# Kernel tuning notes

Hardware: AMD Instinct MI355X
Metric: run time of the kernel (lower is better)

The kernel has to match this reference:

```python
import jax, jax.numpy as jnp
import numpy as np

B, S, OBS, ZD, HID, T, PD = 256, 512, 64, 16, 256, 64, 2
ITERS, ELITES = 4, 64
SMOOTH, STD_FLOOR = 0.25, 0.2
IW, AW, RW = 1.0, 0.5, 1.0


def setup_inputs() -> dict:
    key = jax.random.key(0)
    ks = jax.random.split(key, 32)
    f32 = jnp.float32

    def w(k, shape):
        return jax.random.normal(k, shape, f32) / np.float32(np.sqrt(shape[0]))

    return {
        "s0": jax.random.normal(ks[0], (B, OBS), f32),
        "eps": jax.random.normal(ks[1], (ITERS, B, S, ZD), f32),
        "enc_w1": w(ks[2], (OBS, HID)), "enc_b1": jnp.zeros((HID,), f32),
        "enc_w2": w(ks[3], (HID, HID)), "enc_b2": jnp.zeros((HID,), f32),
        "zmu_w": w(ks[4], (HID, ZD)), "zmu_b": jnp.zeros((ZD,), f32),
        "zls_w": w(ks[5], (HID, ZD)), "zls_b": jnp.zeros((ZD,), f32),
        "mu_w1": w(ks[6], (OBS + ZD, HID)), "mu_b1": jnp.zeros((HID,), f32),
        "mu_w2": w(ks[7], (HID, HID)), "mu_b2": jnp.zeros((HID,), f32),
        "mu_w3": w(ks[8], (HID, T * PD)), "mu_b3": jnp.zeros((T * PD,), f32),
        "sig_w1": w(ks[9], (ZD, HID)), "sig_b1": jnp.zeros((HID,), f32),
        "sig_w2": w(ks[10], (HID, HID)), "sig_b2": jnp.zeros((HID,), f32),
        "sig_w3": w(ks[11], (HID, T * PD)), "sig_b3": jnp.zeros((T * PD,), f32),  # bias zero-init per nn.init.zeros_
        "risk_w1": w(ks[12], (OBS + ZD, HID)), "risk_b1": jnp.zeros((HID,), f32),
        "risk_w2": w(ks[13], (HID, HID)), "risk_b2": jnp.zeros((HID,), f32),
        "risk_w3": w(ks[14], (HID, 1)), "risk_b3": jnp.zeros((1,), f32),
    }


def _cem_bind(s0, eps, enc_w1, enc_b1, enc_w2, enc_b2, zmu_w, zmu_b, zls_w, zls_b,
              mu_w1, mu_b1, mu_w2, mu_b2, mu_w3, mu_b3,
              sig_w1, sig_b1, sig_w2, sig_b2, sig_w3, sig_b3,
              risk_w1, risk_b1, risk_w2, risk_b2, risk_w3, risk_b3):
    relu = jax.nn.relu
    b, obs = s0.shape
    iters, _, s, zd = eps.shape

    # --- TubeNet.encode: q(z|s0) ---
    h = relu(s0 @ enc_w1 + enc_b1)
    h = relu(h @ enc_w2 + enc_b2)
    mu = h @ zmu_w + zmu_b                                   # [B, ZD]
    std = jnp.exp(jnp.clip(h @ zls_w + zls_b, -4.0, 2.0))    # [B, ZD]

    goal = s0[:, 2:4]                                        # extract_goal
    s0e = jnp.broadcast_to(s0[:, None, :], (b, s, obs))      # [B, S, OBS]

    best_score = jnp.full((b,), -jnp.inf, dtype=s0.dtype)
    best_z = mu

    for i in range(iters):  # small fixed CEM iteration count
        z = mu[:, None, :] + std[:, None, :] * eps[i]        # [B, S, ZD]
        x = jnp.concatenate([s0e, z], axis=-1)               # [B, S, OBS+ZD]

        # predict_tube: mu_net(s0, z)
        hm = relu(x @ mu_w1 + mu_b1)
        hm = relu(hm @ mu_w2 + mu_b2)
        mu_out = (hm @ mu_w3 + mu_b3).reshape(b, s, T, PD)

        # sigma_net(z), clamp(-4, 3); agency = -mean(log sigma) = -mean(logsig)
        hs = relu(z @ sig_w1 + sig_b1)
        hs = relu(hs @ sig_w2 + sig_b2)
        logsig = jnp.clip(hs @ sig_w3 + sig_b3, -4.0, 3.0)   # [B, S, T*PD]

        # intent proxy: ||mu_T - goal||^2
        intent = jnp.sum((mu_out[:, :, -1, :] - goal[:, None, :]) ** 2, axis=-1)  # [B, S]
        agency = -jnp.mean(logsig, axis=-1)                  # [B, S]

        # RiskNet(s0, z)
        hr = relu(x @ risk_w1 + risk_b1)
        hr = relu(hr @ risk_w2 + risk_b2)
        risk = jax.nn.sigmoid(hr @ risk_w3 + risk_b3)[..., 0]  # [B, S]

        score = -IW * intent + AW * agency - RW * risk       # [B, S]

        vals, idx = jax.lax.top_k(score, ELITES)             # [B, E]
        elite_z = jnp.take_along_axis(z, idx[:, :, None], axis=1)  # [B, E, ZD]

        better = vals[:, 0] > best_score
        top_z = jnp.take_along_axis(z, idx[:, :1, None], axis=1)[:, 0, :]
        best_score = jnp.where(better, vals[:, 0], best_score)
        best_z = jnp.where(better[:, None], top_z, best_z)

        new_mu = elite_z.mean(axis=1)
        new_std = jnp.std(elite_z, axis=1, ddof=1)           # torch .std default (unbiased)
        mu = SMOOTH * mu + (1.0 - SMOOTH) * new_mu
        std = jnp.maximum(SMOOTH * std + (1.0 - SMOOTH) * new_std, STD_FLOOR)

    return jnp.concatenate([best_z, best_score[:, None]], axis=-1)  # [B, ZD+1]


def reference(s0, eps, enc_w1, enc_b1, enc_w2, enc_b2, zmu_w, zmu_b, zls_w, zls_b,
              mu_w1, mu_b1, mu_w2, mu_b2, mu_w3, mu_b3,
              sig_w1, sig_b1, sig_w2, sig_b2, sig_w3, sig_b3,
              risk_w1, risk_b1, risk_w2, risk_b2, risk_w3, risk_b3):
    return _cem_bind(s0, eps, enc_w1, enc_b1, enc_w2, enc_b2, zmu_w, zmu_b, zls_w, zls_b,
                     mu_w1, mu_b1, mu_w2, mu_b2, mu_w3, mu_b3,
                     sig_w1, sig_b1, sig_w2, sig_b2, sig_w3, sig_b3,
                     risk_w1, risk_b1, risk_w2, risk_b2, risk_w3, risk_b3)
```

## Files before the change

kernel.cpp:

```cpp
#include <hip/hip_runtime.h>

#define B_    256
#define S_    512
#define OBS_  64
#define ZD_   16
#define HID_  256
#define ITERS_ 4
#define RT_   64
#define STRH_ 68

__global__ __launch_bounds__(256) void enc_kernel(
    const float* __restrict__ s0,
    const float* __restrict__ w1, const float* __restrict__ b1,
    const float* __restrict__ w2, const float* __restrict__ b2,
    const float* __restrict__ zmw, const float* __restrict__ zmb,
    const float* __restrict__ zlw, const float* __restrict__ zlb,
    const float* __restrict__ mu_w1, const float* __restrict__ mu_b1,
    const float* __restrict__ risk_w1, const float* __restrict__ risk_b1,
    float* __restrict__ mu, float* __restrict__ stdv, float* __restrict__ bscore,
    float* __restrict__ base_mu, float* __restrict__ base_risk)
{
    __shared__ float s0s[OBS_];
    __shared__ float h1[HID_];
    __shared__ float h2[HID_];
    const int b = blockIdx.x, tid = threadIdx.x;
    if (tid < OBS_) s0s[tid] = s0[b * OBS_ + tid];
    __syncthreads();
    {
        float am = mu_b1[tid], ar = risk_b1[tid];
        for (int k = 0; k < OBS_; ++k) {
            am = fmaf(s0s[k], mu_w1[k * 256 + tid], am);
            ar = fmaf(s0s[k], risk_w1[k * 256 + tid], ar);
        }
        base_mu[b * 256 + tid]   = am;
        base_risk[b * 256 + tid] = ar;
    }
    float a = b1[tid];
    for (int k = 0; k < OBS_; ++k) a = fmaf(s0s[k], w1[k * HID_ + tid], a);
    h1[tid] = fmaxf(a, 0.f);
    __syncthreads();
    float a2 = b2[tid];
    for (int k = 0; k < HID_; ++k) a2 = fmaf(h1[k], w2[k * HID_ + tid], a2);
    h2[tid] = fmaxf(a2, 0.f);
    __syncthreads();
    if (tid < ZD_) {
        float m = zmb[tid];
        for (int k = 0; k < HID_; ++k) m = fmaf(h2[k], zmw[k * ZD_ + tid], m);
        mu[b * ZD_ + tid] = m;
    } else if (tid < 2 * ZD_) {
        const int d = tid - ZD_;
        float l = zlb[d];
        for (int k = 0; k < HID_; ++k) l = fmaf(h2[k], zlw[k * ZD_ + d], l);
        l = fminf(fmaxf(l, -4.f), 2.f);
        stdv[b * ZD_ + d] = expf(l);
    } else if (tid == 2 * ZD_) {
        bscore[b] = -INFINITY;
    }
}

__device__ __forceinline__ void fma32x2(
    const float* __restrict__ row, float wx, float wy,
    float* __restrict__ acc0, float* __restrict__ acc1)
{
#pragma unroll
    for (int s = 0; s < 4; ++s) {
        const float4 a0 = *(const float4*)(row + 8 * s);
        const float4 a1 = *(const float4*)(row + 8 * s + 4);
        const float aa[8] = {a0.x,a0.y,a0.z,a0.w, a1.x,a1.y,a1.z,a1.w};
#pragma unroll
        for (int r = 0; r < 8; ++r) {
            acc0[8*s+r] = fmaf(aa[r], wx, acc0[8*s+r]);
            acc1[8*s+r] = fmaf(aa[r], wy, acc1[8*s+r]);
        }
    }
}

__device__ __forceinline__ void fma32x1(
    const float* __restrict__ row, float w, float* __restrict__ acc)
{
#pragma unroll
    for (int s = 0; s < 4; ++s) {
        const float4 a0 = *(const float4*)(row + 8 * s);
        const float4 a1 = *(const float4*)(row + 8 * s + 4);
        const float aa[8] = {a0.x,a0.y,a0.z,a0.w, a1.x,a1.y,a1.z,a1.w};
#pragma unroll
        for (int r = 0; r < 8; ++r) acc[8*s+r] = fmaf(aa[r], w, acc[8*s+r]);
    }
}

__device__ __forceinline__ void gemm_k2(
    const float* __restrict__ inS, int K,
    const float* __restrict__ wcol,
    float* __restrict__ acc0, float* __restrict__ acc1)
{
    float2 wA[4], wB[4];
#pragma unroll
    for (int i = 0; i < 4; ++i) wA[i] = *(const float2*)(wcol + (size_t)i * 256);
#pragma unroll 1
    for (int k0 = 0; k0 < K; k0 += 8) {
#pragma unroll
        for (int i = 0; i < 4; ++i)
            wB[i] = *(const float2*)(wcol + (size_t)(k0 + 4 + i) * 256);
#pragma unroll
        for (int i = 0; i < 4; ++i)
            fma32x2(inS + (k0 + i) * STRH_, wA[i].x, wA[i].y, acc0, acc1);
        if (k0 + 8 < K) {
#pragma unroll
            for (int i = 0; i < 4; ++i)
                wA[i] = *(const float2*)(wcol + (size_t)(k0 + 8 + i) * 256);
        }
#pragma unroll
        for (int i = 0; i < 4; ++i)
            fma32x2(inS + (k0 + 4 + i) * STRH_, wB[i].x, wB[i].y, acc0, acc1);
    }
}

__device__ __forceinline__ void gemm_k1(
    const float* __restrict__ inS, int K,
    const float* __restrict__ wcol, int wstride, float* __restrict__ acc)
{
    float wA[4], wB[4];
#pragma unroll
    for (int i = 0; i < 4; ++i) wA[i] = wcol[(size_t)i * wstride];
#pragma unroll 1
    for (int k0 = 0; k0 < K; k0 += 8) {
#pragma unroll
        for (int i = 0; i < 4; ++i) wB[i] = wcol[(size_t)(k0 + 4 + i) * wstride];
#pragma unroll
        for (int i = 0; i < 4; ++i) fma32x1(inS + (k0 + i) * STRH_, wA[i], acc);
        if (k0 + 8 < K) {
#pragma unroll
            for (int i = 0; i < 4; ++i) wA[i] = wcol[(size_t)(k0 + 8 + i) * wstride];
        }
#pragma unroll
        for (int i = 0; i < 4; ++i) fma32x1(inS + (k0 + 4 + i) * STRH_, wB[i], acc);
    }
}

__device__ __forceinline__ void store32_relu(float* __restrict__ dst, int c,
                                             int g32, const float* __restrict__ acc)
{
#pragma unroll
    for (int q = 0; q < 8; ++q) {
        float4 o;
        o.x = fmaxf(acc[4*q+0], 0.f); o.y = fmaxf(acc[4*q+1], 0.f);
        o.z = fmaxf(acc[4*q+2], 0.f); o.w = fmaxf(acc[4*q+3], 0.f);
        *(float4*)(dst + (size_t)c * STRH_ + g32 + 4*q) = o;
    }
}

__global__ __launch_bounds__(256, 2) void score_kernel(
    const float* __restrict__ s0, const float* __restrict__ eps,
    const float* __restrict__ mu_w1,
    const float* __restrict__ mu_w2, const float* __restrict__ mu_b2,
    const float* __restrict__ mu_w3, const float* __restrict__ mu_b3,
    const float* __restrict__ sig_w1, const float* __restrict__ sig_b1,
    const float* __restrict__ sig_w2, const float* __restrict__ sig_b2,
    const float* __restrict__ sig_w3, const float* __restrict__ sig_b3,
    const float* __restrict__ risk_w1,
    const float* __restrict__ risk_w2, const float* __restrict__ risk_b2,
    const float* __restrict__ risk_w3, const float* __restrict__ risk_b3,
    const float* __restrict__ base_mu, const float* __restrict__ base_risk,
    const float* __restrict__ mu, const float* __restrict__ stdv,
    float* __restrict__ score, int iter)
{
    __shared__ __align__(16) float zT[ZD_ * STRH_];
    __shared__ __align__(16) float h[HID_ * STRH_];
    __shared__ float red[4][RT_], red2[4][RT_];
    __shared__ float intentL[RT_], agencyL[RT_];
    __shared__ float muS[ZD_], stdS[ZD_];

    const int tid  = threadIdx.x;
    const int g    = tid >> 7;
    const int g32  = g * 32;
    const int c0   = (tid & 127) * 2;
    const int row0 = blockIdx.x * RT_;
    const int b    = row0 >> 9;

    if (tid < ZD_) { muS[tid] = mu[b * ZD_ + tid]; stdS[tid] = stdv[b * ZD_ + tid]; }
    __syncthreads();
    {
        const float* epsI = eps + ((size_t)iter * B_ * S_ + row0) * ZD_;
        for (int l = tid; l < RT_ * ZD_; l += 256) {
            const int r = l >> 4, d = l & 15;
            zT[d * STRH_ + r] = fmaf(stdS[d], epsI[l], muS[d]);
        }
    }
    __syncthreads();

    float acc0[32], acc1[32];

    {
        const float2 bm = *(const float2*)(base_mu + (size_t)b * 256 + c0);
#pragma unroll
        for (int r = 0; r < 32; ++r) { acc0[r] = bm.x; acc1[r] = bm.y; }
        gemm_k2(zT + g32, ZD_, mu_w1 + (size_t)OBS_ * 256 + c0, acc0, acc1);
        store32_relu(h, c0, g32, acc0); store32_relu(h, c0 + 1, g32, acc1);
    }
    __syncthreads();
    {
        const float2 bv = *(const float2*)(mu_b2 + c0);
#pragma unroll
        for (int r = 0; r < 32; ++r) { acc0[r] = bv.x; acc1[r] = bv.y; }
        gemm_k2(h + g32, HID_, mu_w2 + c0, acc0, acc1);
    }
    __syncthreads();
    store32_relu(h, c0, g32, acc0); store32_relu(h, c0 + 1, g32, acc1);
    __syncthreads();
    {
        const int r = tid & 63, seg = tid >> 6;
        float p0 = 0.f, p1 = 0.f;
        for (int i = 0; i < 64; ++i) {
            const int k = seg * 64 + i;
            const float hv = h[k * STRH_ + r];
            const float2 wv = *(const float2*)(mu_w3 + (size_t)k * 128 + 126);
            p0 = fmaf(hv, wv.x, p0);
            p1 = fmaf(hv, wv.y, p1);
        }
        red[seg][r] = p0; red2[seg][r] = p1;
    }
    {
        const float2 bv = *(const float2*)(sig_b1 + c0);
#pragma unroll
        for (int r = 0; r < 32; ++r) { acc0[r] = bv.x; acc1[r] = bv.y; }
        gemm_k2(zT + g32, ZD_, sig_w1 + c0, acc0, acc1);
    }
    __syncthreads();
    store32_relu(h, c0, g32, acc0); store32_relu(h, c0 + 1, g32, acc1);
    if (tid < RT_) {
        float m0 = red[0][tid] + red[1][tid] + red[2][tid] + red[3][tid] + mu_b3[126];
        float m1 = red2[0][tid] + red2[1][tid] + red2[2][tid] + red2[3][tid] + mu_b3[127];
        const float g0 = s0[b * OBS_ + 2], g1 = s0[b * OBS_ + 3];
        const float d0 = m0 - g0, d1 = m1 - g1;
        intentL[tid] = d0 * d0 + d1 * d1;
    }
    __syncthreads();
    {
        const float2 bv = *(const float2*)(sig_b2 + c0);
#pragma unroll
        for (int r = 0; r < 32; ++r) { acc0[r] = bv.x; acc1[r] = bv.y; }
        gemm_k2(h + g32, HID_, sig_w2 + c0, acc0, acc1);
    }
    __syncthreads();
    store32_relu(h, c0, g32, acc0); store32_relu(h, c0 + 1, g32, acc1);
    __syncthreads();
    {
        const int c = tid & 127;
        float acc[32];
        const float bv = sig_b3[c];
#pragma unroll
        for (int r = 0; r < 32; ++r) acc[r] = bv;
        gemm_k1(h + g32, HID_, sig_w3 + c, 128, acc);
        __syncthreads();
#pragma unroll
        for (int q = 0; q < 8; ++q) {
            float4 o;
            o.x = fminf(fmaxf(acc[4*q+0], -4.f), 3.f);
            o.y = fminf(fmaxf(acc[4*q+1], -4.f), 3.f);
            o.z = fminf(fmaxf(acc[4*q+2], -4.f), 3.f);
            o.w = fminf(fmaxf(acc[4*q+3], -4.f), 3.f);
            *(float4*)(h + (size_t)c * STRH_ + g32 + 4*q) = o;
        }
    }
    __syncthreads();
    {
        const int r = tid & 63, seg = tid >> 6;
        float s = 0.f;
        for (int i = 0; i < 32; ++i) s += h[(seg * 32 + i) * STRH_ + r];
        red[seg][r] = s;
    }
    {
        const float2 bm = *(const float2*)(base_risk + (size_t)b * 256 + c0);
#pragma unroll
        for (int r = 0; r < 32; ++r) { acc0[r] = bm.x; acc1[r] = bm.y; }
        gemm_k2(zT + g32, ZD_, risk_w1 + (size_t)OBS_ * 256 + c0, acc0, acc1);
    }
    __syncthreads();
    store32_relu(h, c0, g32, acc0); store32_relu(h, c0 + 1, g32, acc1);
    if (tid < RT_) {
        const float s = red[0][tid] + red[1][tid] + red[2][tid] + red[3][tid];
        agencyL[tid] = -s * (1.f / 128.f);
    }
    __syncthreads();
    {
        const float2 bv = *(const float2*)(risk_b2 + c0);
#pragma unroll
        for (int r = 0; r < 32; ++r) { acc0[r] = bv.x; acc1[r] = bv.y; }
        gemm_k2(h + g32, HID_, risk_w2 + c0, acc0, acc1);
    }
    __syncthreads();
    store32_relu(h, c0, g32, acc0); store32_relu(h, c0 + 1, g32, acc1);
    __syncthreads();
    {
        const int r = tid & 63, seg = tid >> 6;
        float p = 0.f;
        for (int i = 0; i < 64; ++i) {
            const int k = seg * 64 + i;
            p = fmaf(h[k * STRH_ + r], risk_w3[k], p);
        }
        red[seg][r] = p;
    }
    __syncthreads();
    if (tid < RT_) {
        const float p = red[0][tid] + red[1][tid] + red[2][tid] + red[3][tid];
        const float risk = 1.f / (1.f + expf(-(p + risk_b3[0])));
        score[row0 + tid] = -intentL[tid] + 0.5f * agencyL[tid] - risk;
    }
}

__global__ __launch_bounds__(256) void update_kernel(
    const float* __restrict__ score, const float* __restrict__ eps,
    float* __restrict__ mu, float* __restrict__ stdv,
    float* __restrict__ bscore, float* __restrict__ bz, int iter)
{
    __shared__ unsigned long long keys[512];
    __shared__ float ez[64][ZD_];
    __shared__ float mold[ZD_], sold[ZD_];
    __shared__ int flagL, idx0L;

    const int b = blockIdx.x, tid = threadIdx.x;

    for (int l = tid; l < 512; l += 256) {
        const float sc = score[b * 512 + l];
        unsigned int u = __float_as_uint(sc);
        u = (u & 0x80000000u) ? ~u : (u | 0x80000000u);
        const unsigned long long key =
            ((unsigned long long)u << 32) | (unsigned long long)(511 - l);
        keys[l] = ~key;
    }
    if (tid < ZD_) { mold[tid] = mu[b * ZD_ + tid]; sold[tid] = stdv[b * ZD_ + tid]; }
    __syncthreads();

    for (int size = 2; size < 512; size <<= 1) {
        const int ddd = ((tid & (size >> 1)) != 0) ? 0 : 1;
        for (int stride = size >> 1; stride > 0; stride >>= 1) {
            __syncthreads();
            const int pos = 2 * tid - (tid & (stride - 1));
            const unsigned long long a = keys[pos], c = keys[pos + stride];
            if ((a > c) == (ddd != 0)) { keys[pos] = c; keys[pos + stride] = a; }
        }
    }
    for (int stride = 256; stride > 0; stride >>= 1) {
        __syncthreads();
        const int pos = 2 * tid - (tid & (stride - 1));
        const unsigned long long a = keys[pos], c = keys[pos + stride];
        if (a > c) { keys[pos] = c; keys[pos + stride] = a; }
    }
    __syncthreads();

    const float* epsB = eps + ((size_t)iter * B_ * S_ + (size_t)b * S_) * ZD_;
    for (int l = tid; l < 64 * ZD_; l += 256) {
        const int e = l >> 4, d = l & 15;
        const unsigned long long key = ~keys[e];
        const int idx = 511 - (int)(key & 0xFFFFFFFFull);
        ez[e][d] = fmaf(sold[d], epsB[idx * ZD_ + d], mold[d]);
    }
    __syncthreads();

    if (tid < ZD_) {
        float s = 0.f;
        for (int e = 0; e < 64; ++e) s += ez[e][tid];
        const float mean = s * (1.f / 64.f);
        float v = 0.f;
        for (int e = 0; e < 64; ++e) { const float d = ez[e][tid] - mean; v = fmaf(d, d, v); }
        const float sd = sqrtf(v * (1.f / 63.f));
        mu[b * ZD_ + tid]   = 0.25f * mold[tid] + 0.75f * mean;
        stdv[b * ZD_ + tid] = fmaxf(0.25f * sold[tid] + 0.75f * sd, 0.2f);
    }
    if (tid == 0) {
        const unsigned long long key = ~keys[0];
        const int idx0 = 511 - (int)(key & 0xFFFFFFFFull);
        const float v = score[b * 512 + idx0];
        const int better = (v > bscore[b]) ? 1 : 0;
        if (better) bscore[b] = v;
        flagL = better; idx0L = idx0;
    }
    __syncthreads();
    if (tid < ZD_ && flagL)
        bz[b * ZD_ + tid] = fmaf(sold[tid], epsB[idx0L * ZD_ + tid], mold[tid]);
}

__global__ __launch_bounds__(256) void out_kernel(
    const float* __restrict__ bz, const float* __restrict__ bscore,
    float* __restrict__ out)
{
    const int i = blockIdx.x * 256 + threadIdx.x;
    if (i < B_ * 17) {
        const int b = i / 17, d = i % 17;
        out[i] = (d < ZD_) ? bz[b * ZD_ + d] : bscore[b];
    }
}

extern "C" void kernel_launch(void* const* d_in, const int* in_sizes, int n_in,
                              void* d_out, int out_size, void* d_ws, size_t ws_size,
                              hipStream_t stream)
{
    (void)in_sizes; (void)n_in; (void)out_size; (void)ws_size;
    const float* s0      = (const float*)d_in[0];
    const float* eps     = (const float*)d_in[1];
    const float* enc_w1  = (const float*)d_in[2];
    const float* enc_b1  = (const float*)d_in[3];
    const float* enc_w2  = (const float*)d_in[4];
    const float* enc_b2  = (const float*)d_in[5];
    const float* zmu_w   = (const float*)d_in[6];
    const float* zmu_b   = (const float*)d_in[7];
    const float* zls_w   = (const float*)d_in[8];
    const float* zls_b   = (const float*)d_in[9];
    const float* mu_w1   = (const float*)d_in[10];
    const float* mu_b1   = (const float*)d_in[11];
    const float* mu_w2   = (const float*)d_in[12];
    const float* mu_b2   = (const float*)d_in[13];
    const float* mu_w3   = (const float*)d_in[14];
    const float* mu_b3   = (const float*)d_in[15];
    const float* sig_w1  = (const float*)d_in[16];
    const float* sig_b1  = (const float*)d_in[17];
    const float* sig_w2  = (const float*)d_in[18];
    const float* sig_b2  = (const float*)d_in[19];
    const float* sig_w3  = (const float*)d_in[20];
    const float* sig_b3  = (const float*)d_in[21];
    const float* risk_w1 = (const float*)d_in[22];
    const float* risk_b1 = (const float*)d_in[23];
    const float* risk_w2 = (const float*)d_in[24];
    const float* risk_b2 = (const float*)d_in[25];
    const float* risk_w3 = (const float*)d_in[26];
    const float* risk_b3 = (const float*)d_in[27];

    float* ws        = (float*)d_ws;
    float* mu        = ws;
    float* stdv      = ws + 4096;
    float* bscore    = ws + 8192;
    float* bz        = ws + 8448;
    float* score     = ws + 12544;
    float* base_mu   = ws + 143616;
    float* base_risk = ws + 209152;

    enc_kernel<<<B_, 256, 0, stream>>>(s0, enc_w1, enc_b1, enc_w2, enc_b2,
                                       zmu_w, zmu_b, zls_w, zls_b,
                                       mu_w1, mu_b1, risk_w1, risk_b1,
                                       mu, stdv, bscore, base_mu, base_risk);
    for (int it = 0; it < ITERS_; ++it) {
        score_kernel<<<(B_ * S_) / RT_, 256, 0, stream>>>(
            s0, eps,
            mu_w1, mu_w2, mu_b2, mu_w3, mu_b3,
            sig_w1, sig_b1, sig_w2, sig_b2, sig_w3, sig_b3,
            risk_w1, risk_w2, risk_b2, risk_w3, risk_b3,
            base_mu, base_risk,
            mu, stdv, score, it);
        update_kernel<<<B_, 256, 0, stream>>>(score, eps, mu, stdv, bscore, bz, it);
    }
    out_kernel<<<(B_ * 17 + 255) / 256, 256, 0, stream>>>(bz, bscore,
                                                          (float*)d_out);
}
```

Measured before the change: 3.207 ms.

## Retile score kernel GEMMs to 8x8 register blocks per thread

Changes each thread's register tile in the score MLP GEMMs from 32 rows by 2 columns to 8 rows by 8 columns, and the last sigma layer from 32x1 to 8x4. This balances shared-memory activation reads against global weight reads, and weights are now loaded as float4. It also stages the mu_w3 goal columns and risk_w3 in shared memory instead of re-reading them from global memory in the reduction loops. The cost is different LDS access patterns, with eight row groups now reading the same h rows, and possibly a changed register footprint.

New measurement: 3.107 ms. -3.1%, faster.

```diff
diff --git a/kernel.cpp b/kernel.cpp
--- a/kernel.cpp
+++ b/kernel.cpp
@@ -58,94 +58,106 @@
     }
 }
 
-__device__ __forceinline__ void fma32x2(
-    const float* __restrict__ row, float wx, float wy,
-    float* __restrict__ acc0, float* __restrict__ acc1)
-{
-#pragma unroll
-    for (int s = 0; s < 4; ++s) {
-        const float4 a0 = *(const float4*)(row + 8 * s);
-        const float4 a1 = *(const float4*)(row + 8 * s + 4);
-        const float aa[8] = {a0.x,a0.y,a0.z,a0.w, a1.x,a1.y,a1.z,a1.w};
-#pragma unroll
-        for (int r = 0; r < 8; ++r) {
-            acc0[8*s+r] = fmaf(aa[r], wx, acc0[8*s+r]);
-            acc1[8*s+r] = fmaf(aa[r], wy, acc1[8*s+r]);
-        }
-    }
-}
-
-__device__ __forceinline__ void fma32x1(
-    const float* __restrict__ row, float w, float* __restrict__ acc)
-{
-#pragma unroll
-    for (int s = 0; s < 4; ++s) {
-        const float4 a0 = *(const float4*)(row + 8 * s);
-        const float4 a1 = *(const float4*)(row + 8 * s + 4);
-        const float aa[8] = {a0.x,a0.y,a0.z,a0.w, a1.x,a1.y,a1.z,a1.w};
-#pragma unroll
-        for (int r = 0; r < 8; ++r) acc[8*s+r] = fmaf(aa[r], w, acc[8*s+r]);
-    }
-}
-
-__device__ __forceinline__ void gemm_k2(
+__device__ __forceinline__ void fma8x8(
+    const float* __restrict__ row, const float4 w0, const float4 w1,
+    float acc[8][8])
+{
+    const float4 q0 = *(const float4*)(row);
+    const float4 q1 = *(const float4*)(row + 4);
+    const float aa[8] = {q0.x,q0.y,q0.z,q0.w, q1.x,q1.y,q1.z,q1.w};
+    const float ww[8] = {w0.x,w0.y,w0.z,w0.w, w1.x,w1.y,w1.z,w1.w};
+#pragma unroll
+    for (int c = 0; c < 8; ++c)
+#pragma unroll
+        for (int r = 0; r < 8; ++r)
+            acc[c][r] = fmaf(aa[r], ww[c], acc[c][r]);
+}
+
+__device__ __forceinline__ void fma8x4(
+    const float* __restrict__ row, const float4 w0, float acc[4][8])
+{
+    const float4 q0 = *(const float4*)(row);
+    const float4 q1 = *(const float4*)(row + 4);
+    const float aa[8] = {q0.x,q0.y,q0.z,q0.w, q1.x,q1.y,q1.z,q1.w};
+    const float ww[4] = {w0.x,w0.y,w0.z,w0.w};
+#pragma unroll
+    for (int c = 0; c < 4; ++c)
+#pragma unroll
+        for (int r = 0; r < 8; ++r)
+            acc[c][r] = fmaf(aa[r], ww[c], acc[c][r]);
+}
+
+__device__ __forceinline__ void gemm_k8(
     const float* __restrict__ inS, int K,
-    const float* __restrict__ wcol,
-    float* __restrict__ acc0, float* __restrict__ acc1)
-{
-    float2 wA[4], wB[4];
-#pragma unroll
-    for (int i = 0; i < 4; ++i) wA[i] = *(const float2*)(wcol + (size_t)i * 256);
+    const float* __restrict__ wcol, float acc[8][8])
+{
+    float4 wA[4][2], wB[4][2];
+#pragma unroll
+    for (int i = 0; i < 4; ++i) {
+        wA[i][0] = *(const float4*)(wcol + (size_t)i * 256);
+        wA[i][1] = *(const float4*)(wcol + (size_t)i * 256 + 4);
+    }
 #pragma unroll 1
     for (int k0 = 0; k0 < K; k0 += 8) {
 #pragma unroll
+        for (int i = 0; i < 4; ++i) {
+            wB[i][0] = *(const float4*)(wcol + (size_t)(k0 + 4 + i) * 256);
+            wB[i][1] = *(const float4*)(wcol + (size_t)(k0 + 4 + i) * 256 + 4);
+        }
+#pragma unroll
         for (int i = 0; i < 4; ++i)
-            wB[i] = *(const float2*)(wcol + (size_t)(k0 + 4 + i) * 256);
+            fma8x8(inS + (k0 + i) * STRH_, wA[i][0], wA[i][1], acc);
+        if (k0 + 8 < K) {
+#pragma unroll
+            for (int i = 0; i < 4; ++i) {
+                wA[i][0] = *(const float4*)(wcol + (size_t)(k0 + 8 + i) * 256);
+                wA[i][1] = *(const float4*)(wcol + (size_t)(k0 + 8 + i) * 256 + 4);
+            }
+        }
 #pragma unroll
         for (int i = 0; i < 4; ++i)
-            fma32x2(inS + (k0 + i) * STRH_, wA[i].x, wA[i].y, acc0, acc1);
-        if (k0 + 8 < K) {
-#pragma unroll
-            for (int i = 0; i < 4; ++i)
-                wA[i] = *(const float2*)(wcol + (size_t)(k0 + 8 + i) * 256);
-        }
-#pragma unroll
-        for (int i = 0; i < 4; ++i)
-            fma32x2(inS + (k0 + 4 + i) * STRH_, wB[i].x, wB[i].y, acc0, acc1);
-    }
-}
-
-__device__ __forceinline__ void gemm_k1(
+            fma8x8(inS + (k0 + 4 + i) * STRH_, wB[i][0], wB[i][1], acc);
+    }
+}
+
+__device__ __forceinline__ void gemm_l3(
     const float* __restrict__ inS, int K,
-    const float* __restrict__ wcol, int wstride, float* __restrict__ acc)
-{
-    float wA[4], wB[4];
-#pragma unroll
-    for (int i = 0; i < 4; ++i) wA[i] = wcol[(size_t)i * wstride];
+    const float* __restrict__ wcol, float acc[4][8])
+{
+    float4 wA[4], wB[4];
+#pragma unroll
+    for (int i = 0; i < 4; ++i) wA[i] = *(const float4*)(wcol + (size_t)i * 128);
 #pragma unroll 1
     for (int k0 = 0; k0 < K; k0 += 8) {
 #pragma unroll
-        for (int i = 0; i < 4; ++i) wB[i] = wcol[(size_t)(k0 + 4 + i) * wstride];
-#pragma unroll
-        for (int i = 0; i < 4; ++i) fma32x1(inS + (k0 + i) * STRH_, wA[i], acc);
+        for (int i = 0; i < 4; ++i)
+            wB[i] = *(const float4*)(wcol + (size_t)(k0 + 4 + i) * 128);
+#pragma unroll
+        for (int i = 0; i < 4; ++i)
+            fma8x4(inS + (k0 + i) * STRH_, wA[i], acc);
         if (k0 + 8 < K) {
 #pragma unroll
-            for (int i = 0; i < 4; ++i) wA[i] = wcol[(size_t)(k0 + 8 + i) * wstride];
-        }
-#pragma unroll
-        for (int i = 0; i < 4; ++i) fma32x1(inS + (k0 + 4 + i) * STRH_, wB[i], acc);
-    }
-}
-
-__device__ __forceinline__ void store32_relu(float* __restrict__ dst, int c,
-                                             int g32, const float* __restrict__ acc)
-{
-#pragma unroll
-    for (int q = 0; q < 8; ++q) {
-        float4 o;
-        o.x = fmaxf(acc[4*q+0], 0.f); o.y = fmaxf(acc[4*q+1], 0.f);
-        o.z = fmaxf(acc[4*q+2], 0.f); o.w = fmaxf(acc[4*q+3], 0.f);
-        *(float4*)(dst + (size_t)c * STRH_ + g32 + 4*q) = o;
+            for (int i = 0; i < 4; ++i)
+                wA[i] = *(const float4*)(wcol + (size_t)(k0 + 8 + i) * 128);
+        }
+#pragma unroll
+        for (int i = 0; i < 4; ++i)
+            fma8x4(inS + (k0 + 4 + i) * STRH_, wB[i], acc);
+    }
+}
+
+__device__ __forceinline__ void store8x8_relu(float* __restrict__ dst, int c0,
+                                              int g8, const float acc[8][8])
+{
+#pragma unroll
+    for (int c = 0; c < 8; ++c) {
+#pragma unroll
+        for (int q = 0; q < 2; ++q) {
+            float4 o;
+            o.x = fmaxf(acc[c][4*q+0], 0.f); o.y = fmaxf(acc[c][4*q+1], 0.f);
+            o.z = fmaxf(acc[c][4*q+2], 0.f); o.w = fmaxf(acc[c][4*q+3], 0.f);
+            *(float4*)(dst + (size_t)(c0 + c) * STRH_ + g8 + 4*q) = o;
+        }
     }
 }
 
@@ -166,18 +178,26 @@
 {
     __shared__ __align__(16) float zT[ZD_ * STRH_];
     __shared__ __align__(16) float h[HID_ * STRH_];
+    __shared__ float w3m[2 * HID_];
+    __shared__ float rw3[HID_];
     __shared__ float red[4][RT_], red2[4][RT_];
     __shared__ float intentL[RT_], agencyL[RT_];
     __shared__ float muS[ZD_], stdS[ZD_];
 
     const int tid  = threadIdx.x;
-    const int g    = tid >> 7;
-    const int g32  = g * 32;
-    const int c0   = (tid & 127) * 2;
+    const int g    = tid >> 5;
+    const int g8   = g * 8;
+    const int ct   = tid & 31;
+    const int c0   = ct * 8;
     const int row0 = blockIdx.x * RT_;
     const int b    = row0 >> 9;
 
     if (tid < ZD_) { muS[tid] = mu[b * ZD_ + tid]; stdS[tid] = stdv[b * ZD_ + tid]; }
+    {
+        const float2 v = *(const float2*)(mu_w3 + (size_t)tid * 128 + 126);
+        w3m[2 * tid] = v.x; w3m[2 * tid + 1] = v.y;
+        rw3[tid] = risk_w3[tid];
+    }
     __syncthreads();
     {
         const float* epsI = eps + ((size_t)iter * B_ * S_ + row0) * ZD_;
@@ -188,24 +208,32 @@
     }
     __syncthreads();
 
-    float acc0[32], acc1[32];
-
-    {
-        const float2 bm = *(const float2*)(base_mu + (size_t)b * 256 + c0);
-#pragma unroll
-        for (int r = 0; r < 32; ++r) { acc0[r] = bm.x; acc1[r] = bm.y; }
-        gemm_k2(zT + g32, ZD_, mu_w1 + (size_t)OBS_ * 256 + c0, acc0, acc1);
-        store32_relu(h, c0, g32, acc0); store32_relu(h, c0 + 1, g32, acc1);
-    }
-    __syncthreads();
-    {
-        const float2 bv = *(const float2*)(mu_b2 + c0);
-#pragma unroll
-        for (int r = 0; r < 32; ++r) { acc0[r] = bv.x; acc1[r] = bv.y; }
-        gemm_k2(h + g32, HID_, mu_w2 + c0, acc0, acc1);
-    }
-    __syncthreads();
-    store32_relu(h, c0, g32, acc0); store32_relu(h, c0 + 1, g32, acc1);
+    float acc[8][8];
+
+    {
+        const float4 b0 = *(const float4*)(base_mu + (size_t)b * 256 + c0);
+        const float4 b1v = *(const float4*)(base_mu + (size_t)b * 256 + c0 + 4);
+        const float bb[8] = {b0.x,b0.y,b0.z,b0.w, b1v.x,b1v.y,b1v.z,b1v.w};
+#pragma unroll
+        for (int c = 0; c < 8; ++c)
+#pragma unroll
+            for (int r = 0; r < 8; ++r) acc[c][r] = bb[c];
+        gemm_k8(zT + g8, ZD_, mu_w1 + (size_t)OBS_ * 256 + c0, acc);
+        store8x8_relu(h, c0, g8, acc);
+    }
+    __syncthreads();
+    {
+        const float4 b0 = *(const float4*)(mu_b2 + c0);
+        const float4 b1v = *(const float4*)(mu_b2 + c0 + 4);
+        const float bb[8] = {b0.x,b0.y,b0.z,b0.w, b1v.x,b1v.y,b1v.z,b1v.w};
+#pragma unroll
+        for (int c = 0; c < 8; ++c)
+#pragma unroll
+            for (int r = 0; r < 8; ++r) acc[c][r] = bb[c];
+        gemm_k8(h + g8, HID_, mu_w2 + c0, acc);
+    }
+    __syncthreads();
+    store8x8_relu(h, c0, g8, acc);
     __syncthreads();
     {
         const int r = tid & 63, seg = tid >> 6;
@@ -213,20 +241,23 @@
         for (int i = 0; i < 64; ++i) {
             const int k = seg * 64 + i;
             const float hv = h[k * STRH_ + r];
-            const float2 wv = *(const float2*)(mu_w3 + (size_t)k * 128 + 126);
-            p0 = fmaf(hv, wv.x, p0);
-            p1 = fmaf(hv, wv.y, p1);
+            p0 = fmaf(hv, w3m[2 * k],     p0);
+            p1 = fmaf(hv, w3m[2 * k + 1], p1);
         }
         red[seg][r] = p0; red2[seg][r] = p1;
     }
     {
-        const float2 bv = *(const float2*)(sig_b1 + c0);
-#pragma unroll
-        for (int r = 0; r < 32; ++r) { acc0[r] = bv.x; acc1[r] = bv.y; }
-        gemm_k2(zT + g32, ZD_, sig_w1 + c0, acc0, acc1);
-    }
-    __syncthreads();
-    store32_relu(h, c0, g32, acc0); store32_relu(h, c0 + 1, g32, acc1);
+        const float4 b0 = *(const float4*)(sig_b1 + c0);
+        const float4 b1v = *(const float4*)(sig_b1 + c0 + 4);
+        const float bb[8] = {b0.x,b0.y,b0.z,b0.w, b1v.x,b1v.y,b1v.z,b1v.w};
+#pragma unroll
+        for (int c = 0; c < 8; ++c)
+#pragma unroll
+            for (int r = 0; r < 8; ++r) acc[c][r] = bb[c];
+        gemm_k8(zT + g8, ZD_, sig_w1 + c0, acc);
+    }
+    __syncthreads();
+    store8x8_relu(h, c0, g8, acc);
     if (tid < RT_) {
         float m0 = red[0][tid] + red[1][tid] + red[2][tid] + red[3][tid] + mu_b3[126];
         float m1 = red2[0][tid] + red2[1][tid] + red2[2][tid] + red2[3][tid] + mu_b3[127];
@@ -236,30 +267,40 @@
     }
     __syncthreads();
     {
-        const float2 bv = *(const float2*)(sig_b2 + c0);
-#pragma unroll
-        for (int r = 0; r < 32; ++r) { acc0[r] = bv.x; acc1[r] = bv.y; }
-        gemm_k2(h + g32, HID_, sig_w2 + c0, acc0, acc1);
-    }
-    __syncthreads();
-    store32_relu(h, c0, g32, acc0); store32_relu(h, c0 + 1, g32, acc1);
-    __syncthreads();
-    {
-        const int c = tid & 127;
-        float acc[32];
-        const float bv = sig_b3[c];
-#pragma unroll
-        for (int r = 0; r < 32; ++r) acc[r] = bv;
-        gemm_k1(h + g32, HID_, sig_w3 + c, 128, acc);
+        const float4 b0 = *(const float4*)(sig_b2 + c0);
+        const float4 b1v = *(const float4*)(sig_b2 + c0 + 4);
+        const float bb[8] = {b0.x,b0.y,b0.z,b0.w, b1v.x,b1v.y,b1v.z,b1v.w};
+#pragma unroll
+        for (int c = 0; c < 8; ++c)
+#pragma unroll
+            for (int r = 0; r < 8; ++r) acc[c][r] = bb[c];
+        gemm_k8(h + g8, HID_, sig_w2 + c0, acc);
+    }
+    __syncthreads();
+    store8x8_relu(h, c0, g8, acc);
+    __syncthreads();
+    {
+        const int c3 = ct * 4;
+        float a3[4][8];
+        const float4 bv = *(const float4*)(sig_b3 + c3);
+        const float bb[4] = {bv.x, bv.y, bv.z, bv.w};
+#pragma unroll
+        for (int c = 0; c < 4; ++c)
+#pragma unroll
+            for (int r = 0; r < 8; ++r) a3[c][r] = bb[c];
+        gemm_l3(h + g8, HID_, sig_w3 + c3, a3);
         __syncthreads();
 #pragma unroll
-        for (int q = 0; q < 8; ++q) {
-            float4 o;
-            o.x = fminf(fmaxf(acc[4*q+0], -4.f), 3.f);
-            o.y = fminf(fmaxf(acc[4*q+1], -4.f), 3.f);
-            o.z = fminf(fmaxf(acc[4*q+2], -4.f), 3.f);
-            o.w = fminf(fmaxf(acc[4*q+3], -4.f), 3.f);
-            *(float4*)(h + (size_t)c * STRH_ + g32 + 4*q) = o;
+        for (int c = 0; c < 4; ++c) {
+#pragma unroll
+            for (int q = 0; q < 2; ++q) {
+                float4 o;
+                o.x = fminf(fmaxf(a3[c][4*q+0], -4.f), 3.f);
+                o.y = fminf(fmaxf(a3[c][4*q+1], -4.f), 3.f);
+                o.z = fminf(fmaxf(a3[c][4*q+2], -4.f), 3.f);
+                o.w = fminf(fmaxf(a3[c][4*q+3], -4.f), 3.f);
+                *(float4*)(h + (size_t)(c3 + c) * STRH_ + g8 + 4*q) = o;
+            }
         }
     }
     __syncthreads();
@@ -270,33 +311,41 @@
         red[seg][r] = s;
     }
     {
-        const float2 bm = *(const float2*)(base_risk + (size_t)b * 256 + c0);
-#pragma unroll
-        for (int r = 0; r < 32; ++r) { acc0[r] = bm.x; acc1[r] = bm.y; }
-        gemm_k2(zT + g32, ZD_, risk_w1 + (size_t)OBS_ * 256 + c0, acc0, acc1);
-    }
-    __syncthreads();
-    store32_relu(h, c0, g32, acc0); store32_relu(h, c0 + 1, g32, acc1);
+        const float4 b0 = *(const float4*)(base_risk + (size_t)b * 256 + c0);
+        const float4 b1v = *(const float4*)(base_risk + (size_t)b * 256 + c0 + 4);
+        const float bb[8] = {b0.x,b0.y,b0.z,b0.w, b1v.x,b1v.y,b1v.z,b1v.w};
+#pragma unroll
+        for (int c = 0; c < 8; ++c)
+#pragma unroll
+            for (int r = 0; r < 8; ++r) acc[c][r] = bb[c];
+        gemm_k8(zT + g8, ZD_, risk_w1 + (size_t)OBS_ * 256 + c0, acc);
+    }
+    __syncthreads();
+    store8x8_relu(h, c0, g8, acc);
     if (tid < RT_) {
         const float s = red[0][tid] + red[1][tid] + red[2][tid] + red[3][tid];
         agencyL[tid] = -s * (1.f / 128.f);
     }
     __syncthreads();
     {
-        const float2 bv = *(const float2*)(risk_b2 + c0);
-#pragma unroll
-        for (int r = 0; r < 32; ++r) { acc0[r] = bv.x; acc1[r] = bv.y; }
-        gemm_k2(h + g32, HID_, risk_w2 + c0, acc0, acc1);
-    }
-    __syncthreads();
-    store32_relu(h, c0, g32, acc0); store32_relu(h, c0 + 1, g32, acc1);
+        const float4 b0 = *(const float4*)(risk_b2 + c0);
+        const float4 b1v = *(const float4*)(risk_b2 + c0 + 4);
+        const float bb[8] = {b0.x,b0.y,b0.z,b0.w, b1v.x,b1v.y,b1v.z,b1v.w};
+#pragma unroll
+        for (int c = 0; c < 8; ++c)
+#pragma unroll
+            for (int r = 0; r < 8; ++r) acc[c][r] = bb[c];
+        gemm_k8(h + g8, HID_, risk_w2 + c0, acc);
+    }
+    __syncthreads();
+    store8x8_relu(h, c0, g8, acc);
     __syncthreads();
     {
         const int r = tid & 63, seg = tid >> 6;
         float p = 0.f;
         for (int i = 0; i < 64; ++i) {
             const int k = seg * 64 + i;
-            p = fmaf(h[k * STRH_ + r], risk_w3[k], p);
+            p = fmaf(h[k * STRH_ + r], rw3[k], p);
         }
         red[seg][r] = p;
     }
```
